# Kernel optimization log

Hardware: AMD Instinct MI355X
Metric: run time of the kernel (lower is better)

The kernel has to match this reference:

```python
import jax, jax.numpy as jnp
import numpy as np

B, C, H, W = 4, 256, 64, 64
RC = 32  # reduced channels = C // reduction


def setup_inputs() -> dict:
    key = jax.random.key(0)
    ks = jax.random.split(key, 5)
    return {
        "x": jax.random.normal(ks[0], (B, C, H, W), dtype=jnp.float32),
        "context": jax.random.normal(ks[1], (B, C, H, W), dtype=jnp.float32),
        "Wq": jax.random.normal(ks[2], (RC, C), dtype=jnp.float32) * 0.02,
        "bq": jnp.zeros((RC,), dtype=jnp.float32),
        "Wk": jax.random.normal(ks[3], (RC, C), dtype=jnp.float32) * 0.02,
        "bk": jnp.zeros((RC,), dtype=jnp.float32),
        "Wv": jax.random.normal(ks[4], (C, C), dtype=jnp.float32) * 0.02,
        "bv": jnp.zeros((C,), dtype=jnp.float32),
        "gamma": jnp.ones((1,), dtype=jnp.float32),
    }


def reference(x, context, Wq, bq, Wk, bk, Wv, bv, gamma):
    b, c, h, w = x.shape
    _, _, hc, wc = context.shape
    n, m = h * w, hc * wc
    xf = x.reshape(b, c, n)          # (B,C,N)
    cf = context.reshape(b, c, m)    # (B,C,M)
    # 1x1 conv projections == per-pixel linear
    q = jnp.einsum('rc,bcn->bnr', Wq, xf) + bq            # (B,N,RC)
    k = jnp.einsum('rc,bcm->brm', Wk, cf) + bk[:, None]   # (B,RC,M)
    v = jnp.einsum('dc,bcm->bdm', Wv, cf) + bv[:, None]   # (B,C,M)
    scale = 1.0 / jnp.sqrt(jnp.asarray(q.shape[-1], dtype=q.dtype))
    attn = jax.nn.softmax(jnp.einsum('bnr,brm->bnm', q, k) * scale, axis=-1)  # (B,N,M)
    out = jnp.einsum('bdm,bnm->bdn', v, attn).reshape(b, c, h, w)
    return gamma * out + x
```

## Files before the change

kernel.cpp:

```cpp
#include <hip/hip_runtime.h>
#include <hip/hip_bf16.h>


#define B_ 4
#define C_ 256
#define N_ 4096
#define M_ 4096
#define SCALE_ 0.17677669529663687f

typedef __bf16 bf16x8 __attribute__((ext_vector_type(8)));
typedef float f32x4 __attribute__((ext_vector_type(4)));

#define AS1 __attribute__((address_space(1)))
#define AS3 __attribute__((address_space(3)))

static __device__ __forceinline__ unsigned short f2bf(float f) {
    unsigned int u = __float_as_uint(f);
    return (unsigned short)((u + 0x7fffu + ((u >> 16) & 1u)) >> 16);
}
static __device__ __forceinline__ unsigned bfpk(float a, float b) {
    return (unsigned)f2bf(a) | ((unsigned)f2bf(b) << 16);
}
static __device__ __forceinline__ float fp8d(unsigned v) {
    unsigned e = (v >> 3) & 15, m = v & 7;
    float f = e ? __uint_as_float(((e + 120u) << 23) | (m << 20))
                : (float)m * 0x1p-9f;
    return (v & 0x80u) ? -f : f;
}
static __device__ __forceinline__ void gload_lds16(const void* g, void* l) {
    __builtin_amdgcn_global_load_lds((const AS1 unsigned int*)g,
                                     (AS3 unsigned int*)l, 16, 0, 0);
}

__global__ __launch_bounds__(256) void prep(
        const float* __restrict__ Wq, const float* __restrict__ Wk,
        const float* __restrict__ Wv, uint4* __restrict__ Wqf,
        uint4* __restrict__ Wkf, uint4* __restrict__ Wvf) {
    int bid = blockIdx.x, t = threadIdx.x;
    const float* W;
    uint4* dst;
    int frag;
    if (bid < 32)      { W = Wv; dst = Wvf; frag = (bid * 256 + t) >> 6; }
    else if (bid < 36) { W = Wq; dst = Wqf; frag = ((bid - 32) * 256 + t) >> 6; }
    else               { W = Wk; dst = Wkf; frag = ((bid - 36) * 256 + t) >> 6; }
    int lane = t & 63, low = lane & 15, q = lane >> 4;
    int fch = frag & 7, fr = frag >> 3;
    const float* wp = W + (size_t)(fr * 16 + low) * C_ + fch * 32 + q * 8;
    float4 w0 = *(const float4*)wp;
    float4 w1 = *(const float4*)(wp + 4);
    uint4 pk = {bfpk(w0.x, w0.y), bfpk(w0.z, w0.w),
                bfpk(w1.x, w1.y), bfpk(w1.z, w1.w)};
    dst[(size_t)frag * 64 + lane] = pk;
}

__global__ __launch_bounds__(256, 2) void fused_proj(
        const float* __restrict__ x, const float* __restrict__ ctx,
        const uint4* __restrict__ Wqf, const uint4* __restrict__ Wkf,
        const uint4* __restrict__ Wvf,
        const float* __restrict__ bq, const float* __restrict__ bk,
        const float* __restrict__ bv,
        unsigned short* __restrict__ Qf, unsigned short* __restrict__ Kf,
        unsigned char* __restrict__ Vf) {
    __shared__ unsigned short X[64][264];
    __shared__ unsigned short Pl[4][16 * 40];
    __shared__ unsigned char  Vw[4][16 * 40];

    int bid = blockIdx.x;
    bool isX = bid >= 256;
    int lb = bid & 255;
    int b = lb >> 6, pt64 = lb & 63;
    const float* __restrict__ in = (isX ? x : ctx) + (size_t)b * C_ * N_ + pt64 * 64;
    int t = threadIdx.x, wg = t >> 6, lane = t & 63;
    int low = lane & 15, q = lane >> 4;

    {
        int pL = lane;
        const float* s0 = in + pL;
#pragma unroll
        for (int ct = 0; ct < 4; ct++) {
            const float* s2 = s0 + (size_t)(ct * 64 + wg * 16) * N_;
            float v[16];
#pragma unroll
            for (int k = 0; k < 16; k++) v[k] = s2[(size_t)k * N_];
#pragma unroll
            for (int k = 0; k < 16; k += 2)
                *(unsigned*)&X[pL][ct * 64 + wg * 16 + k] = bfpk(v[k], v[k + 1]);
        }
    }
    __syncthreads();

    {
        const uint4* __restrict__ Wf = isX ? Wqf : Wkf;
        const float* __restrict__ bias = isX ? bq : bk;
        unsigned short* __restrict__ dst = isX ? Qf : Kf;
        bf16x8 xf[8];
#pragma unroll
        for (int ch = 0; ch < 8; ch++)
            xf[ch] = *(const bf16x8*)&X[wg * 16 + low][ch * 32 + q * 8];
        const f32x4 zero = {0.f, 0.f, 0.f, 0.f};
        f32x4 acc[2] = {zero, zero};
#pragma unroll
        for (int rt = 0; rt < 2; rt++)
#pragma unroll
            for (int ch = 0; ch < 8; ch++) {
                uint4 wv = Wf[(rt * 8 + ch) * 64 + lane];
                acc[rt] = __builtin_amdgcn_mfma_f32_16x16x32_bf16(
                    __builtin_bit_cast(bf16x8, wv), xf[ch], acc[rt], 0, 0, 0);
            }
        unsigned short* Pw = &Pl[wg][0];
#pragma unroll
        for (int rt = 0; rt < 2; rt++) {
            float b0 = bias[rt * 16 + q * 4 + 0], b1 = bias[rt * 16 + q * 4 + 1];
            float b2 = bias[rt * 16 + q * 4 + 2], b3 = bias[rt * 16 + q * 4 + 3];
            uint2 pk = {bfpk(acc[rt][0] + b0, acc[rt][1] + b1),
                        bfpk(acc[rt][2] + b2, acc[rt][3] + b3)};
            *(uint2*)(Pw + low * 40 + rt * 16 + q * 4) = pk;
        }
        uint4 frag = *(const uint4*)(Pw + low * 40 + q * 8);
        ((uint4*)dst)[((size_t)b * 256 + pt64 * 4 + wg) * 64 + lane] = frag;
    }

    if (!isX) {
        int mstep = wg >> 1, dh = wg & 1;
        bf16x8 vfr[2][8];
#pragma unroll
        for (int mt = 0; mt < 2; mt++)
#pragma unroll
            for (int ch = 0; ch < 8; ch++)
                vfr[mt][ch] = *(const bf16x8*)&X[mstep * 32 + mt * 16 + low][ch * 32 + q * 8];
        unsigned char* Vv = &Vw[wg][0];
        int msg = pt64 * 2 + mstep;
        const f32x4 zero = {0.f, 0.f, 0.f, 0.f};
#pragma unroll
        for (int dt8 = 0; dt8 < 8; dt8++) {
            int dt = dh * 8 + dt8;
            f32x4 a0 = zero, a1 = zero;
#pragma unroll
            for (int ch = 0; ch < 8; ch++) {
                uint4 wv = Wvf[(dt * 8 + ch) * 64 + lane];
                bf16x8 wfr = __builtin_bit_cast(bf16x8, wv);
                a0 = __builtin_amdgcn_mfma_f32_16x16x32_bf16(vfr[0][ch], wfr, a0, 0, 0, 0);
                a1 = __builtin_amdgcn_mfma_f32_16x16x32_bf16(vfr[1][ch], wfr, a1, 0, 0, 0);
            }
            float bb = bv[dt * 16 + low];
            unsigned w0 = __builtin_amdgcn_cvt_pk_fp8_f32(a0[0] + bb, a0[1] + bb, 0, false);
            w0 = __builtin_amdgcn_cvt_pk_fp8_f32(a0[2] + bb, a0[3] + bb, w0, true);
            unsigned w1 = __builtin_amdgcn_cvt_pk_fp8_f32(a1[0] + bb, a1[1] + bb, 0, false);
            w1 = __builtin_amdgcn_cvt_pk_fp8_f32(a1[2] + bb, a1[3] + bb, w1, true);
            *(unsigned*)(Vv + low * 40 + q * 4) = w0;
            *(unsigned*)(Vv + low * 40 + 16 + q * 4) = w1;
            uint2 fr = *(const uint2*)(Vv + low * 40 + q * 8);
            ((uint2*)Vf)[(((size_t)b * 128 + msg) * 16 + dt) * 64 + lane] = fr;
        }
    }
}

__global__ __launch_bounds__(256, 3) void attn(
        const unsigned short* __restrict__ Qf, const unsigned short* __restrict__ Kf,
        const unsigned char* __restrict__ Vf, unsigned char* __restrict__ Op,
        float* __restrict__ Lp) {
    __shared__ __align__(16) unsigned char vbuf[2][16384];
    __shared__ __align__(16) unsigned char Pb[2][4][16 * 72];

    int bid = blockIdx.x;
    int v = bid >> 6;
    int ng = bid & 63;
    int b = v / 3;
    int chunk = v - b * 3;
    int I  = (chunk == 0) ? 22 : 21;
    int s0 = (chunk == 0) ? 0 : (chunk == 1 ? 22 : 43);

    int wave = threadIdx.x >> 6, lane = threadIdx.x & 63;
    int q = lane >> 4, low = lane & 15;
    int nt = ng * 4 + wave;

    const uint4* Qp = (const uint4*)Qf;
    const uint4* Kp = (const uint4*)Kf + (size_t)b * 256 * 64;
    const unsigned char* Vp = Vf + (size_t)b * 1048576;

    bf16x8 qa = __builtin_bit_cast(bf16x8, Qp[(size_t)(b * 256 + nt) * 64 + lane]);

    f32x4 acc[4][4];
#pragma unroll
    for (int tt = 0; tt < 4; tt++)
#pragma unroll
        for (int dd = 0; dd < 4; dd++) acc[tt][dd] = (f32x4){0.f, 0.f, 0.f, 0.f};
    float lacc = 0.f;
    const f32x4 zero = {0.f, 0.f, 0.f, 0.f};

    uint4 kv[4];
#pragma unroll
    for (int u = 0; u < 4; u++)
        kv[u] = Kp[(size_t)(s0 * 4 + u) * 64 + lane];
    f32x4 s[4];
#pragma unroll
    for (int u = 0; u < 4; u++)
        s[u] = __builtin_amdgcn_mfma_f32_16x16x32_bf16(
            __builtin_bit_cast(bf16x8, kv[u]), qa, zero, 0, 0, 0);
#pragma unroll
    for (int ii = 0; ii < 4; ii++) {
        int ck = wave * 4 + ii;
        gload_lds16(Vp + (size_t)s0 * 16384 + ck * 1024 + lane * 16,
                    &vbuf[0][0] + ck * 1024 + lane * 16);
    }
    if (I > 1) {
#pragma unroll
        for (int u = 0; u < 4; u++)
            kv[u] = Kp[(size_t)((s0 + 1) * 4 + u) * 64 + lane];
    }
    {
        unsigned char* Pw = &Pb[0][wave][0];
#pragma unroll
        for (int u = 0; u < 4; u++) {
            float p0 = __expf(s[u][0] * SCALE_), p1 = __expf(s[u][1] * SCALE_);
            float p2 = __expf(s[u][2] * SCALE_), p3 = __expf(s[u][3] * SCALE_);
            lacc += p0 + p1 + p2 + p3;
            unsigned w = __builtin_amdgcn_cvt_pk_fp8_f32(p0, p1, 0, false);
            w = __builtin_amdgcn_cvt_pk_fp8_f32(p2, p3, w, true);
            *(unsigned*)(Pw + low * 72 + u * 16 + q * 4) = w;
        }
    }
    __syncthreads();

    for (int i = 0; i < I; i++) {
        int cur = i & 1, nxt = cur ^ 1;
        if (i + 1 < I) {
#pragma unroll
            for (int ii = 0; ii < 4; ii++) {
                int ck = wave * 4 + ii;
                gload_lds16(Vp + (size_t)(s0 + i + 1) * 16384 + ck * 1024 + lane * 16,
                            &vbuf[nxt][0] + ck * 1024 + lane * 16);
            }
#pragma unroll
            for (int u = 0; u < 4; u++)
                s[u] = __builtin_amdgcn_mfma_f32_16x16x32_bf16(
                    __builtin_bit_cast(bf16x8, kv[u]), qa, zero, 0, 0, 0);
            if (i + 2 < I) {
#pragma unroll
                for (int u = 0; u < 4; u++)
                    kv[u] = Kp[(size_t)((s0 + i + 2) * 4 + u) * 64 + lane];
            }
        }

        const unsigned char* vb = &vbuf[cur][0];
        const unsigned char* Pr = &Pb[cur][0][0];
        long pfr[4][2];
#pragma unroll
        for (int tt = 0; tt < 4; tt++) {
            pfr[tt][0] = *(const long*)(Pr + tt * 1152 + low * 72 + q * 8);
            pfr[tt][1] = *(const long*)(Pr + tt * 1152 + low * 72 + 32 + q * 8);
        }
        long vfr[4][2];
#pragma unroll
        for (int dd = 0; dd < 4; dd++) {
            int dt = wave * 4 + dd;
            vfr[dd][0] = *(const long*)(vb + dt * 512 + lane * 8);
            vfr[dd][1] = *(const long*)(vb + 8192 + dt * 512 + lane * 8);
        }
#pragma unroll
        for (int tt = 0; tt < 4; tt++)
#pragma unroll
            for (int dd = 0; dd < 4; dd++) {
                acc[tt][dd] = __builtin_amdgcn_mfma_f32_16x16x32_fp8_fp8(
                    vfr[dd][0], pfr[tt][0], acc[tt][dd], 0, 0, 0);
                acc[tt][dd] = __builtin_amdgcn_mfma_f32_16x16x32_fp8_fp8(
                    vfr[dd][1], pfr[tt][1], acc[tt][dd], 0, 0, 0);
            }

        if (i + 1 < I) {
            unsigned char* Pw = &Pb[nxt][wave][0];
#pragma unroll
            for (int u = 0; u < 4; u++) {
                float p0 = __expf(s[u][0] * SCALE_), p1 = __expf(s[u][1] * SCALE_);
                float p2 = __expf(s[u][2] * SCALE_), p3 = __expf(s[u][3] * SCALE_);
                lacc += p0 + p1 + p2 + p3;
                unsigned w = __builtin_amdgcn_cvt_pk_fp8_f32(p0, p1, 0, false);
                w = __builtin_amdgcn_cvt_pk_fp8_f32(p2, p3, w, true);
                *(unsigned*)(Pw + low * 72 + u * 16 + q * 4) = w;
            }
        }
        __syncthreads();
    }

    lacc += __shfl_xor(lacc, 16, 64);
    lacc += __shfl_xor(lacc, 32, 64);
    if (lane < 16)
        Lp[(size_t)v * 4096 + nt * 16 + lane] = lacc;

    unsigned* Odw = (unsigned*)&vbuf[0][0];
#pragma unroll
    for (int tt = 0; tt < 4; tt++)
#pragma unroll
        for (int dd = 0; dd < 4; dd++) {
            unsigned w = __builtin_amdgcn_cvt_pk_fp8_f32(acc[tt][dd][0], acc[tt][dd][1], 0, false);
            w = __builtin_amdgcn_cvt_pk_fp8_f32(acc[tt][dd][2], acc[tt][dd][3], w, true);
            Odw[(tt * 16 + low) * 68 + wave * 16 + dd * 4 + q] = w;
        }
    __syncthreads();
    {
        int n = threadIdx.x >> 2, c4 = threadIdx.x & 3;
        size_t rb = ((size_t)v * 4096 + ng * 64 + n) * 256;
#pragma unroll
        for (int k = 0; k < 4; k++)
            *(uint4*)(Op + rb + c4 * 64 + k * 16) =
                *(const uint4*)&Odw[n * 68 + c4 * 16 + k * 4];
    }
}

__global__ __launch_bounds__(256) void combine(
        const unsigned char* __restrict__ Op, const float* __restrict__ Lp,
        const float* __restrict__ x, const float* __restrict__ gamma,
        float* __restrict__ out) {
    __shared__ float W[32][260];
    int bid = blockIdx.x;
    int b = bid >> 7, n0 = (bid & 127) * 32;
    int t = threadIdx.x;
    float g = gamma[0];
    {
        int d4 = t & 63, nn = t >> 6;
#pragma unroll
        for (int rr = 0; rr < 8; rr++) {
            int n = rr * 4 + nn;
            float o0 = 0.f, o1 = 0.f, o2 = 0.f, o3 = 0.f, l = 0.f;
#pragma unroll
            for (int p = 0; p < 3; p++) {
                size_t base = (size_t)(b * 3 + p) * 4096 + n0 + n;
                unsigned pv = *(const unsigned*)(Op + base * 256 + d4 * 4);
                o0 += fp8d(pv & 255u); o1 += fp8d((pv >> 8) & 255u);
                o2 += fp8d((pv >> 16) & 255u); o3 += fp8d(pv >> 24);
                l += Lp[base];
            }
            float sc = g / l;
            f32x4 w = {o0 * sc, o1 * sc, o2 * sc, o3 * sc};
            *(f32x4*)&W[n][d4 * 4] = w;
        }
    }
    __syncthreads();
    {
        int d = t;
        size_t rb = ((size_t)b * 256 + d) * 4096 + n0;
#pragma unroll
        for (int k = 0; k < 8; k++) {
            f32x4 xv = *(const f32x4*)(x + rb + k * 4);
            f32x4 res;
#pragma unroll
            for (int r = 0; r < 4; r++) res[r] = W[k * 4 + r][d] + xv[r];
            *(f32x4*)(out + rb + k * 4) = res;
        }
    }
}

extern "C" void kernel_launch(void* const* d_in, const int* in_sizes, int n_in,
                              void* d_out, int out_size, void* d_ws, size_t ws_size,
                              hipStream_t stream) {
    const float* x     = (const float*)d_in[0];
    const float* ctx   = (const float*)d_in[1];
    const float* Wq    = (const float*)d_in[2];
    const float* bq    = (const float*)d_in[3];
    const float* Wk    = (const float*)d_in[4];
    const float* bk    = (const float*)d_in[5];
    const float* Wv    = (const float*)d_in[6];
    const float* bv    = (const float*)d_in[7];
    const float* gamma = (const float*)d_in[8];
    float* out = (float*)d_out;

    unsigned short* Qf = (unsigned short*)d_ws;
    unsigned short* Kf = Qf + (size_t)B_ * N_ * 32;
    unsigned char*  Vf = (unsigned char*)(Kf + (size_t)B_ * M_ * 32);
    uint4* Wqf = (uint4*)(Vf + (size_t)B_ * M_ * C_);
    uint4* Wkf = Wqf + 16 * 64;
    uint4* Wvf = Wkf + 16 * 64;
    unsigned char* Op = (unsigned char*)(Wvf + 128 * 64);
    float* Lp = (float*)(Op + (size_t)3 * B_ * N_ * C_);

    prep<<<40, 256, 0, stream>>>(Wq, Wk, Wv, Wqf, Wkf, Wvf);
    fused_proj<<<512, 256, 0, stream>>>(x, ctx, Wqf, Wkf, Wvf, bq, bk, bv, Qf, Kf, Vf);
    attn<<<768, 256, 0, stream>>>(Qf, Kf, Vf, Op, Lp);
    combine<<<512, 256, 0, stream>>>(Op, Lp, x, gamma, out);
}
```

Before: 151.8 us.

## Use 32x32x64 scaled fp8 MFMA for the P·V accumulation

Replaces the sixteen pairs of 16x16x32 fp8 MFMAs per iteration with four 32x32x64 mfma_scale f8f6f4 instructions, one per 2x2 block of 32x32 output tiles. The V and P fragment loads and the output write-back are remapped to match the larger tile's lane layout, and the P LDS row stride is padded from 72 to 80 bytes so 16-byte loads stay aligned. The goal is fewer MFMA issues and fewer LDS fragment loads for the same work. The cost is more complex index mapping and a risk of LDS bank conflicts or layout mistakes.

```diff
diff --git a/kernel.cpp b/kernel.cpp
--- a/kernel.cpp
+++ b/kernel.cpp
@@ -10,6 +10,8 @@
 
 typedef __bf16 bf16x8 __attribute__((ext_vector_type(8)));
 typedef float f32x4 __attribute__((ext_vector_type(4)));
+typedef float f32x16 __attribute__((ext_vector_type(16)));
+typedef int i32x8 __attribute__((ext_vector_type(8)));
 
 #define AS1 __attribute__((address_space(1)))
 #define AS3 __attribute__((address_space(3)))
@@ -160,7 +162,7 @@
         const unsigned char* __restrict__ Vf, unsigned char* __restrict__ Op,
         float* __restrict__ Lp) {
     __shared__ __align__(16) unsigned char vbuf[2][16384];
-    __shared__ __align__(16) unsigned char Pb[2][4][16 * 72];
+    __shared__ __align__(16) unsigned char Pb[2][4][16 * 80];
 
     int bid = blockIdx.x;
     int v = bid >> 6;
@@ -172,6 +174,8 @@
 
     int wave = threadIdx.x >> 6, lane = threadIdx.x & 63;
     int q = lane >> 4, low = lane & 15;
+    int hi = lane >> 5;
+    int dsel = q & 1;
     int nt = ng * 4 + wave;
 
     const uint4* Qp = (const uint4*)Qf;
@@ -180,11 +184,11 @@
 
     bf16x8 qa = __builtin_bit_cast(bf16x8, Qp[(size_t)(b * 256 + nt) * 64 + lane]);
 
-    f32x4 acc[4][4];
-#pragma unroll
-    for (int tt = 0; tt < 4; tt++)
-#pragma unroll
-        for (int dd = 0; dd < 4; dd++) acc[tt][dd] = (f32x4){0.f, 0.f, 0.f, 0.f};
+    f32x16 acc2[2][2];
+#pragma unroll
+    for (int tp = 0; tp < 2; tp++)
+#pragma unroll
+        for (int dg = 0; dg < 2; dg++) acc2[tp][dg] = (f32x16)(0.f);
     float lacc = 0.f;
     const f32x4 zero = {0.f, 0.f, 0.f, 0.f};
 
@@ -217,7 +221,7 @@
             lacc += p0 + p1 + p2 + p3;
             unsigned w = __builtin_amdgcn_cvt_pk_fp8_f32(p0, p1, 0, false);
             w = __builtin_amdgcn_cvt_pk_fp8_f32(p2, p3, w, true);
-            *(unsigned*)(Pw + low * 72 + u * 16 + q * 4) = w;
+            *(unsigned*)(Pw + low * 80 + u * 16 + q * 4) = w;
         }
     }
     __syncthreads();
@@ -244,28 +248,27 @@
 
         const unsigned char* vb = &vbuf[cur][0];
         const unsigned char* Pr = &Pb[cur][0][0];
-        long pfr[4][2];
-#pragma unroll
-        for (int tt = 0; tt < 4; tt++) {
-            pfr[tt][0] = *(const long*)(Pr + tt * 1152 + low * 72 + q * 8);
-            pfr[tt][1] = *(const long*)(Pr + tt * 1152 + low * 72 + 32 + q * 8);
-        }
-        long vfr[4][2];
-#pragma unroll
-        for (int dd = 0; dd < 4; dd++) {
-            int dt = wave * 4 + dd;
-            vfr[dd][0] = *(const long*)(vb + dt * 512 + lane * 8);
-            vfr[dd][1] = *(const long*)(vb + 8192 + dt * 512 + lane * 8);
-        }
-#pragma unroll
-        for (int tt = 0; tt < 4; tt++)
-#pragma unroll
-            for (int dd = 0; dd < 4; dd++) {
-                acc[tt][dd] = __builtin_amdgcn_mfma_f32_16x16x32_fp8_fp8(
-                    vfr[dd][0], pfr[tt][0], acc[tt][dd], 0, 0, 0);
-                acc[tt][dd] = __builtin_amdgcn_mfma_f32_16x16x32_fp8_fp8(
-                    vfr[dd][1], pfr[tt][1], acc[tt][dd], 0, 0, 0);
-            }
+        i32x8 vf[2];
+#pragma unroll
+        for (int dg = 0; dg < 2; dg++) {
+            int dt = wave * 4 + dg * 2 + dsel;
+            const unsigned char* vp = vb + hi * 8192 + dt * 512 + low * 8;
+            long* dqw = (long*)&vf[dg];
+#pragma unroll
+            for (int ss = 0; ss < 4; ss++)
+                dqw[ss] = *(const long*)(vp + ss * 128);
+        }
+#pragma unroll
+        for (int tp = 0; tp < 2; tp++) {
+            const unsigned char* pr = Pr + (tp * 2 + dsel) * 1280 + low * 80 + hi * 32;
+            i32x8 pf;
+            ((uint4*)&pf)[0] = *(const uint4*)pr;
+            ((uint4*)&pf)[1] = *(const uint4*)(pr + 16);
+#pragma unroll
+            for (int dg = 0; dg < 2; dg++)
+                acc2[tp][dg] = __builtin_amdgcn_mfma_scale_f32_32x32x64_f8f6f4(
+                    vf[dg], pf, acc2[tp][dg], 0, 0, 0, 127, 0, 127);
+        }
 
         if (i + 1 < I) {
             unsigned char* Pw = &Pb[nxt][wave][0];
@@ -276,7 +279,7 @@
                 lacc += p0 + p1 + p2 + p3;
                 unsigned w = __builtin_amdgcn_cvt_pk_fp8_f32(p0, p1, 0, false);
                 w = __builtin_amdgcn_cvt_pk_fp8_f32(p2, p3, w, true);
-                *(unsigned*)(Pw + low * 72 + u * 16 + q * 4) = w;
+                *(unsigned*)(Pw + low * 80 + u * 16 + q * 4) = w;
             }
         }
         __syncthreads();
@@ -288,14 +291,19 @@
         Lp[(size_t)v * 4096 + nt * 16 + lane] = lacc;
 
     unsigned* Odw = (unsigned*)&vbuf[0][0];
-#pragma unroll
-    for (int tt = 0; tt < 4; tt++)
-#pragma unroll
-        for (int dd = 0; dd < 4; dd++) {
-            unsigned w = __builtin_amdgcn_cvt_pk_fp8_f32(acc[tt][dd][0], acc[tt][dd][1], 0, false);
-            w = __builtin_amdgcn_cvt_pk_fp8_f32(acc[tt][dd][2], acc[tt][dd][3], w, true);
-            Odw[(tt * 16 + low) * 68 + wave * 16 + dd * 4 + q] = w;
-        }
+    int l31 = lane & 31;
+#pragma unroll
+    for (int tp = 0; tp < 2; tp++)
+#pragma unroll
+        for (int dg = 0; dg < 2; dg++)
+#pragma unroll
+            for (int k = 0; k < 4; k++) {
+                unsigned w = __builtin_amdgcn_cvt_pk_fp8_f32(
+                    acc2[tp][dg][4 * k + 0], acc2[tp][dg][4 * k + 1], 0, false);
+                w = __builtin_amdgcn_cvt_pk_fp8_f32(
+                    acc2[tp][dg][4 * k + 2], acc2[tp][dg][4 * k + 3], w, true);
+                Odw[(tp * 32 + l31) * 68 + wave * 16 + dg * 8 + k * 2 + hi] = w;
+            }
     __syncthreads();
     {
         int n = threadIdx.x >> 2, c4 = threadIdx.x & 3;
```

Measured after the change: 150.1 us. About the same (-1.1%).
